# Kernel tuning notes

Measured on AMD Instinct MI355X. Metric: run time of the kernel, lower is better.

Reference implementation:

```python
import jax, jax.numpy as jnp
import numpy as np

D_MODEL = 768
N_HEADS = 12
D_FF = 3072
EPS = 1e-5


def _layernorm(x, g, b):
    mu = jnp.mean(x, axis=-1, keepdims=True)
    var = jnp.mean(jnp.square(x - mu), axis=-1, keepdims=True)
    return (x - mu) * jax.lax.rsqrt(var + EPS) * g + b


def setup_inputs() -> dict:
    key = jax.random.key(0)
    ks = jax.random.split(key, 16)
    d, f = D_MODEL, D_FF
    s = 1.0 / np.sqrt(d)
    inp = {
        "x": jax.random.normal(ks[0], (1, 4096, d), dtype=jnp.float32),
        "Wq": jax.random.normal(ks[1], (d, d), dtype=jnp.float32) * s,
        "bq": jnp.zeros((d,), jnp.float32),
        "Wk": jax.random.normal(ks[2], (d, d), dtype=jnp.float32) * s,
        "bk": jnp.zeros((d,), jnp.float32),
        "Wv": jax.random.normal(ks[3], (d, d), dtype=jnp.float32) * s,
        "bv": jnp.zeros((d,), jnp.float32),
        "Wo": jax.random.normal(ks[4], (d, d), dtype=jnp.float32) * s,
        "bo": jnp.zeros((d,), jnp.float32),
        "ln1_g": jnp.ones((d,), jnp.float32),
        "ln1_b": jnp.zeros((d,), jnp.float32),
        "ln2_g": jnp.ones((d,), jnp.float32),
        "ln2_b": jnp.zeros((d,), jnp.float32),
        "W1": jax.random.normal(ks[5], (d, f), dtype=jnp.float32) * s,
        "b1": jnp.zeros((f,), jnp.float32),
        "W2": jax.random.normal(ks[6], (f, d), dtype=jnp.float32) * (1.0 / np.sqrt(f)),
        "b2": jnp.zeros((d,), jnp.float32),
    }
    return inp


def reference(x, Wq, bq, Wk, bk, Wv, bv, Wo, bo, ln1_g, ln1_b, ln2_g, ln2_b, W1, b1, W2, b2):
    b, s, d = x.shape
    h = N_HEADS
    dk = d // h

    # --- attention sublayer (pre-norm residual) ---
    xn = _layernorm(x, ln1_g, ln1_b)

    def proj(W, bias):
        y = xn @ W + bias                      # [b, s, d]
        return y.reshape(b, s, h, dk).transpose(0, 2, 1, 3)  # [b, h, s, dk]

    q, k, v = proj(Wq, bq), proj(Wk, bk), proj(Wv, bv)
    scores = jnp.einsum("bhqd,bhkd->bhqk", q, k) / np.sqrt(dk)
    attn = jax.nn.softmax(scores, axis=-1)
    ctx = jnp.einsum("bhqk,bhkd->bhqd", attn, v)
    ctx = ctx.transpose(0, 2, 1, 3).reshape(b, s, d)
    x = x + (ctx @ Wo + bo)

    # --- FFN sublayer (pre-norm residual) ---
    xn2 = _layernorm(x, ln2_g, ln2_b)
    ff = jax.nn.gelu(xn2 @ W1 + b1, approximate=False) @ W2 + b2
    return x + ff
```

## Files before the change

kernel.cpp:

```cpp
#include <hip/hip_runtime.h>
#include <hip/hip_bf16.h>

typedef __attribute__((ext_vector_type(8))) __bf16 bf16x8;
typedef __attribute__((ext_vector_type(4))) __bf16 bf16x4;
typedef __attribute__((ext_vector_type(4))) float f32x4;
typedef __attribute__((ext_vector_type(4))) unsigned short u16x4;
typedef unsigned short ushort_t;

__device__ __forceinline__ ushort_t f2bf(float f) {
    union { float f; unsigned u; } v; v.f = f;
    unsigned r = v.u + 0x7fffu + ((v.u >> 16) & 1u);
    return (ushort_t)(r >> 16);
}

__device__ __forceinline__ void gload16(const ushort_t* g, ushort_t* l) {
    __builtin_amdgcn_global_load_lds(
        (const __attribute__((address_space(1))) unsigned int*)g,
        (__attribute__((address_space(3))) unsigned int*)l,
        16, 0, 0);
}

__device__ __forceinline__ void ln_row(const float* __restrict__ xr,
                                       const float* __restrict__ g,
                                       const float* __restrict__ b,
                                       ushort_t* __restrict__ orow, int t) {
    float v0 = xr[t], v1 = xr[t + 256], v2 = xr[t + 512];
    float s  = v0 + v1 + v2;
    float s2 = v0 * v0 + v1 * v1 + v2 * v2;
#pragma unroll
    for (int off = 32; off; off >>= 1) {
        s  += __shfl_down(s, off);
        s2 += __shfl_down(s2, off);
    }
    __shared__ float red[8];
    const int wid = t >> 6, lane = t & 63;
    if (lane == 0) { red[wid] = s; red[4 + wid] = s2; }
    __syncthreads();
    __shared__ float stats[2];
    if (t == 0) {
        float S = red[0] + red[1] + red[2] + red[3];
        float S2 = red[4] + red[5] + red[6] + red[7];
        float mu = S * (1.0f / 768.0f);
        float var = S2 * (1.0f / 768.0f) - mu * mu;
        stats[0] = mu;
        stats[1] = rsqrtf(var + 1e-5f);
    }
    __syncthreads();
    const float mu = stats[0], rs = stats[1];
    orow[t]       = f2bf((v0 - mu) * rs * g[t]       + b[t]);
    orow[t + 256] = f2bf((v1 - mu) * rs * g[t + 256] + b[t + 256]);
    orow[t + 512] = f2bf((v2 - mu) * rs * g[t + 512] + b[t + 512]);
}

__global__ __launch_bounds__(256) void ln_kernel(const float* __restrict__ x,
                                                 const float* __restrict__ g,
                                                 const float* __restrict__ b,
                                                 ushort_t* __restrict__ out) {
    const int row = blockIdx.x;
    ln_row(x + (size_t)row * 768, g, b, out + (size_t)row * 768, threadIdx.x);
}

__global__ __launch_bounds__(256) void prep_ln(
    const float* __restrict__ Wq, const float* __restrict__ Wk,
    const float* __restrict__ Wv, const float* __restrict__ Wo,
    const float* __restrict__ W1, const float* __restrict__ W2,
    const float* __restrict__ bq, const float* __restrict__ bk,
    const float* __restrict__ bv,
    const float* __restrict__ x, const float* __restrict__ ln1_g,
    const float* __restrict__ ln1_b,
    ushort_t* __restrict__ WqkvT, ushort_t* __restrict__ WoT,
    ushort_t* __restrict__ W1T, ushort_t* __restrict__ W2T,
    float* __restrict__ bqkv, ushort_t* __restrict__ xn) {
    const int bid = blockIdx.x;
    const int t = threadIdx.x;
    if (bid >= 6915) {
        const int row = bid - 6915;
        ln_row(x + (size_t)row * 768, ln1_g, ln1_b, xn + (size_t)row * 768, t);
        return;
    }
    if (bid >= 6912) {
        const int i = bid - 6912;
        const float* s = (i == 0) ? bq : (i == 1) ? bk : bv;
#pragma unroll
        for (int j = t; j < 768; j += 256) bqkv[i * 768 + j] = s[j];
        return;
    }
    const float* src; ushort_t* dst; int R, C, ti;
    if (bid < 576)       { src = Wq; dst = WqkvT;               R = 768;  C = 768;  ti = bid; }
    else if (bid < 1152) { src = Wk; dst = WqkvT + 768 * 768;   R = 768;  C = 768;  ti = bid - 576; }
    else if (bid < 1728) { src = Wv; dst = WqkvT + 2 * 768 * 768; R = 768; C = 768; ti = bid - 1152; }
    else if (bid < 2304) { src = Wo; dst = WoT;                 R = 768;  C = 768;  ti = bid - 1728; }
    else if (bid < 4608) { src = W1; dst = W1T;                 R = 768;  C = 3072; ti = bid - 2304; }
    else                 { src = W2; dst = W2T;                 R = 3072; C = 768;  ti = bid - 4608; }
    const int tpr = C >> 5;
    const int c0 = (ti % tpr) * 32, r0 = (ti / tpr) * 32;
    __shared__ float tile[32][33];
    {
        const int c = t & 31, r = t >> 5;
#pragma unroll
        for (int i = 0; i < 4; i++)
            tile[r + i * 8][c] = src[(size_t)(r0 + r + i * 8) * C + c0 + c];
    }
    __syncthreads();
    {
        const int oc = t >> 3, q = t & 7;
        u16x4 o;
#pragma unroll
        for (int k = 0; k < 4; k++) o[k] = f2bf(tile[q * 4 + k][oc]);
        *(u16x4*)&dst[(size_t)(c0 + oc) * R + r0 + q * 4] = o;
    }
}

template <int BN, int GELU, int RES, int OUTF, int OUTB, int OUTV>
__global__ __launch_bounds__(256, 3)
void gemm_bt(const ushort_t* __restrict__ A, const ushort_t* __restrict__ Bt,
             const float* __restrict__ bias, const float* __restrict__ res,
             float* __restrict__ outF, ushort_t* __restrict__ outB, int ldo,
             ushort_t* __restrict__ outV,
             int M, int N, int K) {
    constexpr int TR  = 128 + BN;
    constexpr int LL  = TR / 64;
    constexpr int WCF = BN / 32;
    __shared__ __align__(16) ushort_t Ls[2][TR * 32];

    const int nbx = gridDim.x;
    const int nwg = nbx * gridDim.y;
    int fb = blockIdx.y * nbx + blockIdx.x;
    fb = (fb & 7) * (nwg >> 3) + (fb >> 3);
    const int m0 = (fb / nbx) * 128, n0 = (fb % nbx) * BN;

    const int t = threadIdx.x;
    const int wid = t >> 6, lane = t & 63;
    const int wr = wid >> 1, wc = wid & 1;
    const int row16 = lane & 15, kg = lane >> 4;
    const int kb = kg * 8;

    const int srow = lane >> 2, scol = (lane & 3) * 8;
    const ushort_t* gsrc[LL];
    int lofs[LL];
#pragma unroll
    for (int i = 0; i < LL; i++) {
        const int r0 = wid * (TR / 4) + 16 * i;
        gsrc[i] = (r0 < 128 ? A + (size_t)(m0 + r0 + srow) * K
                            : Bt + (size_t)(n0 + r0 - 128 + srow) * K) + scol;
        lofs[i] = r0 * 32;
    }

#define STAGE(buf, kofs) do {                                        \
        _Pragma("unroll")                                            \
        for (int i = 0; i < LL; i++)                                 \
            gload16(gsrc[i] + (kofs), &Ls[buf][lofs[i]]);            \
    } while (0)

    f32x4 acc[4][WCF] = {};
    const int NS = K >> 5;
    STAGE(0, 0);
    STAGE(1, 32);
    int cur = 0;

    for (int s = 0; s < NS; ++s) {
        if (s + 1 == NS) asm volatile("s_waitcnt vmcnt(0)" ::: "memory");
        else             asm volatile("s_waitcnt vmcnt(%0)" :: "i"(LL) : "memory");
        __builtin_amdgcn_s_barrier();

        bf16x8 a[4], b[WCF];
#pragma unroll
        for (int i = 0; i < 4; i++)
            a[i] = *(const bf16x8*)&Ls[cur][(wr * 64 + i * 16 + row16) * 32 + kb];
#pragma unroll
        for (int j = 0; j < WCF; j++)
            b[j] = *(const bf16x8*)&Ls[cur][(128 + wc * (BN / 2) + j * 16 + row16) * 32 + kb];
        asm volatile("s_waitcnt lgkmcnt(0)" ::: "memory");
        __builtin_amdgcn_s_barrier();
        if (s + 2 < NS) STAGE(cur, (s + 2) * 32);

        __builtin_amdgcn_s_setprio(1);
#pragma unroll
        for (int i = 0; i < 4; i++)
#pragma unroll
            for (int j = 0; j < WCF; j++)
                acc[i][j] = __builtin_amdgcn_mfma_f32_16x16x32_bf16(a[i], b[j], acc[i][j], 0, 0, 0);
        __builtin_amdgcn_s_setprio(0);
        cur ^= 1;
    }
#undef STAGE

#pragma unroll
    for (int i = 0; i < 4; i++)
#pragma unroll
        for (int j = 0; j < WCF; j++) {
            const int col = n0 + wc * (BN / 2) + j * 16 + row16;
            const float bv = bias[col];
            const int rb = m0 + wr * 64 + i * 16 + kg * 4;
            if (OUTV && col >= 1536) {
                bf16x4 pk;
#pragma unroll
                for (int r = 0; r < 4; r++) pk[r] = (__bf16)(acc[i][j][r] + bv);
                *(bf16x4*)&outV[(size_t)(col - 1536) * 4096 + rb] = pk;
            } else {
#pragma unroll
                for (int r = 0; r < 4; r++) {
                    const int row = rb + r;
                    float v = acc[i][j][r] + bv;
                    if (GELU) {
                        float u = v + 0.044715f * v * v * v;
                        float e = __builtin_amdgcn_exp2f(2.30220779f * u);
                        v = v * e * __builtin_amdgcn_rcpf(e + 1.0f);
                    }
                    if (RES) v += res[(size_t)row * N + col];
                    if (OUTF) outF[(size_t)row * N + col] = v;
                    if (OUTB) outB[(size_t)row * ldo + col] = f2bf(v);
                }
            }
        }
}

__device__ __forceinline__ int swz(int row, int col) {
    return row * 64 + (col ^ ((row & 7) << 3));
}

__global__ __launch_bounds__(256, 3)
void attn_kernel(const ushort_t* __restrict__ qk,
                 const ushort_t* __restrict__ Vt,
                 ushort_t* __restrict__ ctx) {
    int fb = blockIdx.y * 64 + blockIdx.x;
    fb = (fb & 7) * 96 + (fb >> 3);
    const int q0 = (fb & 63) * 64;
    const int h  = fb >> 6;

    const int t  = threadIdx.x;
    const int w = t >> 6, lane = t & 63;
    const int row16 = lane & 15, kg = lane >> 4;
    const int kb = kg * 8;

    __shared__ __align__(16) ushort_t Qs[64 * 64];
    __shared__ __align__(16) ushort_t Ks[2][64 * 64];
    __shared__ __align__(16) ushort_t Vs[2][64 * 64];
    ushort_t* Ps = Qs;

    const int sr = t >> 2, sc = (t & 3) * 8;

    {
        const size_t qb = (size_t)(q0 + sr) * 1536 + h * 64 + sc;
        *(uint4*)&Qs[swz(sr, sc)]      = *(const uint4*)&qk[qb];
        *(uint4*)&Qs[swz(sr, sc + 32)] = *(const uint4*)&qk[qb + 32];
        const size_t kbase = (size_t)sr * 1536 + 768 + h * 64 + sc;
        *(uint4*)&Ks[0][swz(sr, sc)]      = *(const uint4*)&qk[kbase];
        *(uint4*)&Ks[0][swz(sr, sc + 32)] = *(const uint4*)&qk[kbase + 32];
        const size_t vbase = (size_t)(h * 64 + sr) * 4096 + sc;
        *(uint4*)&Vs[0][swz(sr, sc)]      = *(const uint4*)&Vt[vbase];
        *(uint4*)&Vs[0][swz(sr, sc + 32)] = *(const uint4*)&Vt[vbase + 32];
    }
    const bf16x8 qa0 = *(const bf16x8*)&Qs[swz(w * 16 + row16, kb)];
    const bf16x8 qa1 = *(const bf16x8*)&Qs[swz(w * 16 + row16, 32 + kb)];
    __syncthreads();

    const int rr = lane >> 3;
    const int gcol = ((lane & 7) ^ rr) * 8;
    const ushort_t* gK = qk + 768 + h * 64 + gcol + (size_t)(w * 16 + rr) * 1536;
    const ushort_t* gV = Vt + (size_t)(h * 64 + w * 16 + rr) * 4096 + gcol;

    bf16x8 vones;
#pragma unroll
    for (int i = 0; i < 8; i++) vones[i] = (__bf16)1.0f;

    f32x4 o_acc[4] = {};
    f32x4 o_l = {};
    int cur = 0;
    const float SC = 0.18033688011112042f;

    for (int it = 0; it < 64; ++it) {
        if (it != 63) {
            const int kv1 = (it + 1) * 64;
            ushort_t* kd = &Ks[cur ^ 1][w * 1024];
            ushort_t* vd = &Vs[cur ^ 1][w * 1024];
            gload16(gK + (size_t)kv1 * 1536,       kd);
            gload16(gK + (size_t)(kv1 + 8) * 1536, kd + 512);
            gload16(gV + kv1,                      vd);
            gload16(gV + kv1 + 8 * 4096,           vd + 512);
        }

        const ushort_t* Kc = Ks[cur];
        const ushort_t* Vc = Vs[cur];

        f32x4 s_acc[4];
        __builtin_amdgcn_s_setprio(1);
#pragma unroll
        for (int f = 0; f < 4; f++) {
            bf16x8 ka0 = *(const bf16x8*)&Kc[swz(f * 16 + row16, kb)];
            bf16x8 ka1 = *(const bf16x8*)&Kc[swz(f * 16 + row16, 32 + kb)];
            f32x4 z = {};
            z = __builtin_amdgcn_mfma_f32_16x16x32_bf16(ka0, qa0, z, 0, 0, 0);
            s_acc[f] = __builtin_amdgcn_mfma_f32_16x16x32_bf16(ka1, qa1, z, 0, 0, 0);
        }
        __builtin_amdgcn_s_setprio(0);

#pragma unroll
        for (int f = 0; f < 4; f++) {
            bf16x4 pk;
#pragma unroll
            for (int r = 0; r < 4; r++)
                pk[r] = (__bf16)__builtin_amdgcn_exp2f(fminf(s_acc[f][r] * SC, 30.0f));
            *(bf16x4*)&Ps[swz(w * 16 + row16, f * 16 + kg * 4)] = pk;
        }

        const bf16x8 pa0 = *(const bf16x8*)&Ps[swz(w * 16 + row16, kb)];
        const bf16x8 pa1 = *(const bf16x8*)&Ps[swz(w * 16 + row16, 32 + kb)];
        __builtin_amdgcn_s_setprio(1);
#pragma unroll
        for (int f = 0; f < 4; f++) {
            bf16x8 vb0 = *(const bf16x8*)&Vc[swz(f * 16 + row16, kb)];
            bf16x8 vb1 = *(const bf16x8*)&Vc[swz(f * 16 + row16, 32 + kb)];
            o_acc[f] = __builtin_amdgcn_mfma_f32_16x16x32_bf16(pa0, vb0, o_acc[f], 0, 0, 0);
            o_acc[f] = __builtin_amdgcn_mfma_f32_16x16x32_bf16(pa1, vb1, o_acc[f], 0, 0, 0);
        }
        o_l = __builtin_amdgcn_mfma_f32_16x16x32_bf16(pa0, vones, o_l, 0, 0, 0);
        o_l = __builtin_amdgcn_mfma_f32_16x16x32_bf16(pa1, vones, o_l, 0, 0, 0);
        __builtin_amdgcn_s_setprio(0);

        __syncthreads();
        cur ^= 1;
    }

#pragma unroll
    for (int f = 0; f < 4; f++)
#pragma unroll
        for (int r = 0; r < 4; r++) {
            const int qrow = q0 + w * 16 + kg * 4 + r;
            ctx[(size_t)qrow * 768 + h * 64 + f * 16 + row16] = f2bf(o_acc[f][r] / o_l[r]);
        }
}

extern "C" void kernel_launch(void* const* d_in, const int* in_sizes, int n_in,
                              void* d_out, int out_size, void* d_ws, size_t ws_size,
                              hipStream_t stream) {
    const float* x     = (const float*)d_in[0];
    const float* Wq    = (const float*)d_in[1];
    const float* bq    = (const float*)d_in[2];
    const float* Wk    = (const float*)d_in[3];
    const float* bk    = (const float*)d_in[4];
    const float* Wv    = (const float*)d_in[5];
    const float* bv    = (const float*)d_in[6];
    const float* Wo    = (const float*)d_in[7];
    const float* bo    = (const float*)d_in[8];
    const float* ln1_g = (const float*)d_in[9];
    const float* ln1_b = (const float*)d_in[10];
    const float* ln2_g = (const float*)d_in[11];
    const float* ln2_b = (const float*)d_in[12];
    const float* W1    = (const float*)d_in[13];
    const float* b1    = (const float*)d_in[14];
    const float* W2    = (const float*)d_in[15];
    const float* b2    = (const float*)d_in[16];

    char* ws = (char*)d_ws;
    ushort_t* WqkvT = (ushort_t*)ws; ws += (size_t)2304 * 768 * 2;
    ushort_t* WoT   = (ushort_t*)ws; ws += (size_t)768 * 768 * 2;
    ushort_t* W1T   = (ushort_t*)ws; ws += (size_t)3072 * 768 * 2;
    ushort_t* W2T   = (ushort_t*)ws; ws += (size_t)768 * 3072 * 2;
    float*    bqkv  = (float*)ws;    ws += (size_t)2304 * 4;
    ushort_t* xn    = (ushort_t*)ws; ws += (size_t)4096 * 768 * 2;
    ushort_t* qk    = (ushort_t*)ws; ws += (size_t)4096 * 1536 * 2;
    ushort_t* Vtb   = (ushort_t*)ws; ws += (size_t)768 * 4096 * 2;
    ushort_t* ctxb  = (ushort_t*)ws; ws += (size_t)4096 * 768 * 2;
    float*    x1    = (float*)ws;    ws += (size_t)4096 * 768 * 4;
    ushort_t* H     = qk;

    prep_ln<<<6915 + 4096, 256, 0, stream>>>(Wq, Wk, Wv, Wo, W1, W2, bq, bk, bv,
                                             x, ln1_g, ln1_b,
                                             WqkvT, WoT, W1T, W2T, bqkv, xn);

    gemm_bt<128, 0, 0, 0, 1, 1><<<dim3(18, 32), 256, 0, stream>>>(
        xn, WqkvT, bqkv, nullptr, nullptr, qk, 1536, Vtb, 4096, 2304, 768);

    attn_kernel<<<dim3(64, 12), 256, 0, stream>>>(qk, Vtb, ctxb);

    gemm_bt<64, 0, 1, 1, 0, 0><<<dim3(12, 32), 256, 0, stream>>>(
        ctxb, WoT, bo, x, x1, nullptr, 0, nullptr, 4096, 768, 768);

    ln_kernel<<<4096, 256, 0, stream>>>(x1, ln2_g, ln2_b, xn);
    gemm_bt<128, 1, 0, 0, 1, 0><<<dim3(24, 32), 256, 0, stream>>>(
        xn, W1T, b1, nullptr, nullptr, H, 3072, nullptr, 4096, 3072, 768);
    gemm_bt<64, 0, 1, 1, 0, 0><<<dim3(12, 32), 256, 0, stream>>>(
        H, W2T, b2, x1, (float*)d_out, nullptr, 0, nullptr, 4096, 768, 3072);

    (void)in_sizes; (void)n_in; (void)out_size; (void)ws_size;
}
```

Measured before the change: 205.5 us.

## Double query tile per attention block to reuse K/V tiles across two subtiles

Each attention workgroup now covers 128 query rows instead of 64, with each wave computing two 16-row query subtiles against every K/V tile loaded into shared memory. K fragments are loaded into registers once and reused for both subtiles, so K/V global and LDS traffic per query row is halved. The cost is a grid of 384 blocks instead of 768, lower occupancy (launch bounds drop from 3 to 2 blocks per CU), and more registers per thread for the doubled accumulators.

```diff
diff --git a/kernel.cpp b/kernel.cpp
--- a/kernel.cpp
+++ b/kernel.cpp
@@ -219,31 +219,33 @@
     return row * 64 + (col ^ ((row & 7) << 3));
 }
 
-__global__ __launch_bounds__(256, 3)
+__global__ __launch_bounds__(256, 2)
 void attn_kernel(const ushort_t* __restrict__ qk,
                  const ushort_t* __restrict__ Vt,
                  ushort_t* __restrict__ ctx) {
-    int fb = blockIdx.y * 64 + blockIdx.x;
-    fb = (fb & 7) * 96 + (fb >> 3);
-    const int q0 = (fb & 63) * 64;
-    const int h  = fb >> 6;
+    int fb = blockIdx.y * 32 + blockIdx.x;
+    fb = (fb & 7) * 48 + (fb >> 3);
+    const int q0 = (fb & 31) * 128;
+    const int h  = fb >> 5;
 
     const int t  = threadIdx.x;
     const int w = t >> 6, lane = t & 63;
     const int row16 = lane & 15, kg = lane >> 4;
     const int kb = kg * 8;
 
-    __shared__ __align__(16) ushort_t Qs[64 * 64];
+    __shared__ __align__(16) ushort_t Ps[128 * 64];
     __shared__ __align__(16) ushort_t Ks[2][64 * 64];
     __shared__ __align__(16) ushort_t Vs[2][64 * 64];
-    ushort_t* Ps = Qs;
-
-    const int sr = t >> 2, sc = (t & 3) * 8;
 
     {
-        const size_t qb = (size_t)(q0 + sr) * 1536 + h * 64 + sc;
-        *(uint4*)&Qs[swz(sr, sc)]      = *(const uint4*)&qk[qb];
-        *(uint4*)&Qs[swz(sr, sc + 32)] = *(const uint4*)&qk[qb + 32];
+        const int qr = t >> 1, cb = (t & 1) * 32;
+        const size_t qbase = (size_t)(q0 + qr) * 1536 + h * 64 + cb;
+#pragma unroll
+        for (int j = 0; j < 4; j++)
+            *(uint4*)&Ps[swz(qr, cb + j * 8)] = *(const uint4*)&qk[qbase + j * 8];
+    }
+    {
+        const int sr = t >> 2, sc = (t & 3) * 8;
         const size_t kbase = (size_t)sr * 1536 + 768 + h * 64 + sc;
         *(uint4*)&Ks[0][swz(sr, sc)]      = *(const uint4*)&qk[kbase];
         *(uint4*)&Ks[0][swz(sr, sc + 32)] = *(const uint4*)&qk[kbase + 32];
@@ -251,8 +253,12 @@
         *(uint4*)&Vs[0][swz(sr, sc)]      = *(const uint4*)&Vt[vbase];
         *(uint4*)&Vs[0][swz(sr, sc + 32)] = *(const uint4*)&Vt[vbase + 32];
     }
-    const bf16x8 qa0 = *(const bf16x8*)&Qs[swz(w * 16 + row16, kb)];
-    const bf16x8 qa1 = *(const bf16x8*)&Qs[swz(w * 16 + row16, 32 + kb)];
+    bf16x8 qa0[2], qa1[2];
+#pragma unroll
+    for (int qb = 0; qb < 2; qb++) {
+        qa0[qb] = *(const bf16x8*)&Ps[swz(w * 32 + qb * 16 + row16, kb)];
+        qa1[qb] = *(const bf16x8*)&Ps[swz(w * 32 + qb * 16 + row16, 32 + kb)];
+    }
     __syncthreads();
 
     const int rr = lane >> 3;
@@ -264,8 +270,8 @@
 #pragma unroll
     for (int i = 0; i < 8; i++) vones[i] = (__bf16)1.0f;
 
-    f32x4 o_acc[4] = {};
-    f32x4 o_l = {};
+    f32x4 o_acc[2][4] = {};
+    f32x4 o_l[2] = {};
     int cur = 0;
     const float SC = 0.18033688011112042f;
 
@@ -283,39 +289,58 @@
         const ushort_t* Kc = Ks[cur];
         const ushort_t* Vc = Vs[cur];
 
-        f32x4 s_acc[4];
+        bf16x8 ka0[4], ka1[4];
+#pragma unroll
+        for (int f = 0; f < 4; f++) {
+            ka0[f] = *(const bf16x8*)&Kc[swz(f * 16 + row16, kb)];
+            ka1[f] = *(const bf16x8*)&Kc[swz(f * 16 + row16, 32 + kb)];
+        }
+
+        f32x4 s_acc[2][4];
         __builtin_amdgcn_s_setprio(1);
 #pragma unroll
-        for (int f = 0; f < 4; f++) {
-            bf16x8 ka0 = *(const bf16x8*)&Kc[swz(f * 16 + row16, kb)];
-            bf16x8 ka1 = *(const bf16x8*)&Kc[swz(f * 16 + row16, 32 + kb)];
-            f32x4 z = {};
-            z = __builtin_amdgcn_mfma_f32_16x16x32_bf16(ka0, qa0, z, 0, 0, 0);
-            s_acc[f] = __builtin_amdgcn_mfma_f32_16x16x32_bf16(ka1, qa1, z, 0, 0, 0);
-        }
+        for (int qb = 0; qb < 2; qb++)
+#pragma unroll
+            for (int f = 0; f < 4; f++) {
+                f32x4 z = {};
+                z = __builtin_amdgcn_mfma_f32_16x16x32_bf16(ka0[f], qa0[qb], z, 0, 0, 0);
+                s_acc[qb][f] = __builtin_amdgcn_mfma_f32_16x16x32_bf16(ka1[f], qa1[qb], z, 0, 0, 0);
+            }
         __builtin_amdgcn_s_setprio(0);
 
 #pragma unroll
-        for (int f = 0; f < 4; f++) {
-            bf16x4 pk;
-#pragma unroll
-            for (int r = 0; r < 4; r++)
-                pk[r] = (__bf16)__builtin_amdgcn_exp2f(fminf(s_acc[f][r] * SC, 30.0f));
-            *(bf16x4*)&Ps[swz(w * 16 + row16, f * 16 + kg * 4)] = pk;
-        }
-
-        const bf16x8 pa0 = *(const bf16x8*)&Ps[swz(w * 16 + row16, kb)];
-        const bf16x8 pa1 = *(const bf16x8*)&Ps[swz(w * 16 + row16, 32 + kb)];
+        for (int qb = 0; qb < 2; qb++)
+#pragma unroll
+            for (int f = 0; f < 4; f++) {
+                bf16x4 pk;
+#pragma unroll
+                for (int r = 0; r < 4; r++)
+                    pk[r] = (__bf16)__builtin_amdgcn_exp2f(fminf(s_acc[qb][f][r] * SC, 30.0f));
+                *(bf16x4*)&Ps[swz(w * 32 + qb * 16 + row16, f * 16 + kg * 4)] = pk;
+            }
+
+        bf16x8 pa0[2], pa1[2];
+#pragma unroll
+        for (int qb = 0; qb < 2; qb++) {
+            pa0[qb] = *(const bf16x8*)&Ps[swz(w * 32 + qb * 16 + row16, kb)];
+            pa1[qb] = *(const bf16x8*)&Ps[swz(w * 32 + qb * 16 + row16, 32 + kb)];
+        }
         __builtin_amdgcn_s_setprio(1);
 #pragma unroll
         for (int f = 0; f < 4; f++) {
             bf16x8 vb0 = *(const bf16x8*)&Vc[swz(f * 16 + row16, kb)];
             bf16x8 vb1 = *(const bf16x8*)&Vc[swz(f * 16 + row16, 32 + kb)];
-            o_acc[f] = __builtin_amdgcn_mfma_f32_16x16x32_bf16(pa0, vb0, o_acc[f], 0, 0, 0);
-            o_acc[f] = __builtin_amdgcn_mfma_f32_16x16x32_bf16(pa1, vb1, o_acc[f], 0, 0, 0);
-        }
-        o_l = __builtin_amdgcn_mfma_f32_16x16x32_bf16(pa0, vones, o_l, 0, 0, 0);
-        o_l = __builtin_amdgcn_mfma_f32_16x16x32_bf16(pa1, vones, o_l, 0, 0, 0);
+#pragma unroll
+            for (int qb = 0; qb < 2; qb++) {
+                o_acc[qb][f] = __builtin_amdgcn_mfma_f32_16x16x32_bf16(pa0[qb], vb0, o_acc[qb][f], 0, 0, 0);
+                o_acc[qb][f] = __builtin_amdgcn_mfma_f32_16x16x32_bf16(pa1[qb], vb1, o_acc[qb][f], 0, 0, 0);
+            }
+        }
+#pragma unroll
+        for (int qb = 0; qb < 2; qb++) {
+            o_l[qb] = __builtin_amdgcn_mfma_f32_16x16x32_bf16(pa0[qb], vones, o_l[qb], 0, 0, 0);
+            o_l[qb] = __builtin_amdgcn_mfma_f32_16x16x32_bf16(pa1[qb], vones, o_l[qb], 0, 0, 0);
+        }
         __builtin_amdgcn_s_setprio(0);
 
         __syncthreads();
@@ -323,12 +348,15 @@
     }
 
 #pragma unroll
-    for (int f = 0; f < 4; f++)
-#pragma unroll
-        for (int r = 0; r < 4; r++) {
-            const int qrow = q0 + w * 16 + kg * 4 + r;
-            ctx[(size_t)qrow * 768 + h * 64 + f * 16 + row16] = f2bf(o_acc[f][r] / o_l[r]);
-        }
+    for (int qb = 0; qb < 2; qb++)
+#pragma unroll
+        for (int f = 0; f < 4; f++)
+#pragma unroll
+            for (int r = 0; r < 4; r++) {
+                const int qrow = q0 + w * 32 + qb * 16 + kg * 4 + r;
+                ctx[(size_t)qrow * 768 + h * 64 + f * 16 + row16] =
+                    f2bf(o_acc[qb][f][r] / o_l[qb][r]);
+            }
 }
 
 extern "C" void kernel_launch(void* const* d_in, const int* in_sizes, int n_in,
@@ -372,7 +400,7 @@
     gemm_bt<128, 0, 0, 0, 1, 1><<<dim3(18, 32), 256, 0, stream>>>(
         xn, WqkvT, bqkv, nullptr, nullptr, qk, 1536, Vtb, 4096, 2304, 768);
 
-    attn_kernel<<<dim3(64, 12), 256, 0, stream>>>(qk, Vtb, ctxb);
+    attn_kernel<<<dim3(32, 12), 256, 0, stream>>>(qk, Vtb, ctxb);
 
     gemm_bt<64, 0, 1, 1, 0, 0><<<dim3(12, 32), 256, 0, stream>>>(
         ctxb, WoT, bo, x, x1, nullptr, 0, nullptr, 4096, 768, 768);
```

Measured after the change: 222.5 us. 8.2% more time.
